# Performance work log

Hardware: AMD Instinct MI355X
Metric: run time of the kernel (lower is better)

Reference implementation:

```python
import jax, jax.numpy as jnp
import numpy as np

S, D_MODEL, H, D_K, D_V = 2048, 1024, 16, 64, 64


def setup_inputs() -> dict:
    key = jax.random.key(0)
    ks = jax.random.split(key, 10)
    sd = 0.02
    return {
        "embeddings": jax.random.normal(ks[0], (S, D_MODEL), dtype=jnp.float32),
        # per-head projection weights (torch Linear: y = x @ W.T + b; here stored as [h, d_in, d_out])
        "Wq": jax.random.normal(ks[1], (H, D_MODEL, D_K), dtype=jnp.float32) * sd,
        "bq": jax.random.normal(ks[2], (H, D_K), dtype=jnp.float32) * sd,
        "Wk": jax.random.normal(ks[3], (H, D_MODEL, D_K), dtype=jnp.float32) * sd,
        "bk": jax.random.normal(ks[4], (H, D_K), dtype=jnp.float32) * sd,
        "Wv": jax.random.normal(ks[5], (H, D_MODEL, D_V), dtype=jnp.float32) * sd,
        "bv": jax.random.normal(ks[6], (H, D_V), dtype=jnp.float32) * sd,
        "Wo": jax.random.normal(ks[7], (H * D_V, D_MODEL), dtype=jnp.float32) * sd,
        "bo": jax.random.normal(ks[8], (D_MODEL,), dtype=jnp.float32) * sd,
    }


def reference(embeddings, Wq, bq, Wk, bk, Wv, bv, Wo, bo):
    # Batched equivalent of the per-head Python loop of ScaledDotProductAttention layers.
    # q,k: [h, s, d_k]; v: [h, s, d_v]
    q = jnp.einsum('sd,hdk->hsk', embeddings, Wq) + bq[:, None, :]
    k = jnp.einsum('sd,hdk->hsk', embeddings, Wk) + bk[:, None, :]
    v = jnp.einsum('sd,hdv->hsv', embeddings, Wv) + bv[:, None, :]
    scale = jnp.asarray(1.0 / np.sqrt(q.shape[-1]), q.dtype)
    scores = jnp.einsum('hsk,htk->hst', q, k) * scale  # [h, s, s]
    attn = jax.nn.softmax(scores, axis=-1)
    heads = jnp.einsum('hst,htv->hsv', attn, v)  # [h, s, d_v]
    # torch.cat(results, dim=1): head outputs concatenated along feature dim -> [s, h*d_v]
    concat = jnp.transpose(heads, (1, 0, 2)).reshape(embeddings.shape[0], -1)
    return concat @ Wo + bo
```

## Files before the change

### kernel.cpp

```cpp
#include <hip/hip_runtime.h>
#include <hip/hip_bf16.h>

typedef unsigned short u16;
typedef __attribute__((ext_vector_type(8))) short bf16x8;
typedef __attribute__((ext_vector_type(4))) float f32x4;

#define S_LEN 2048
#define NH 16

__device__ __forceinline__ u16 f2bf(float x) {
  union { float f; unsigned u; } v; v.f = x;
  unsigned r = v.u + 0x7fffu + ((v.u >> 16) & 1u);
  return (u16)(r >> 16);
}

__device__ __forceinline__ unsigned cvtpk_bf16(float lo, float hi) {
  unsigned w;
  asm("v_cvt_pk_bf16_f32 %0, %1, %2" : "=v"(w) : "v"(lo), "v"(hi));
  return w;
}

__device__ __forceinline__ void async16(const void* g, void* l) {
  __builtin_amdgcn_global_load_lds(
      (const __attribute__((address_space(1))) unsigned int*)g,
      (__attribute__((address_space(3))) unsigned int*)l, 16, 0, 0);
}

__device__ __forceinline__ f32x4 mfma16(bf16x8 a, bf16x8 b, f32x4 c) {
  return __builtin_amdgcn_mfma_f32_16x16x32_bf16(a, b, c, 0, 0, 0);
}

#define QSCALE (0.125f * 1.44269504089f)

__global__ __launch_bounds__(256) void convert_kernel(
    const float* __restrict__ emb, const float* __restrict__ Wq,
    const float* __restrict__ Wk, const float* __restrict__ Wv,
    const float* __restrict__ bq, const float* __restrict__ bk,
    const float* __restrict__ bv, const float* __restrict__ Wo,
    u16* __restrict__ emb_bf, u16* __restrict__ wqkv_t,
    u16* __restrict__ wo_t, float* __restrict__ bqkv) {
  __shared__ float lds[64][65];
  const int b = blockIdx.x, tid = threadIdx.x;
  if (b < 2048) {
    int i = b * 1024 + tid * 4;
    float4 v = *(const float4*)(emb + i);
    ushort4 o = {f2bf(v.x), f2bf(v.y), f2bf(v.z), f2bf(v.w)};
    *(ushort4*)(emb_bf + i) = o;
    return;
  }
  if (b < 2816) {
    int tt = b - 2048;
    int kind = tt >> 8;
    int rem = tt & 255;
    int h = rem >> 4, k0 = (rem & 15) << 6;
    const float* W = (kind == 0) ? Wq : ((kind == 1) ? Wk : Wv);
    const float* src = W + ((size_t)h * 1024 + k0) * 64;
#pragma unroll
    for (int rr = 0; rr < 4; ++rr) {
      int k = rr * 16 + (tid >> 4);
      int d4 = (tid & 15) << 2;
      float4 v = *(const float4*)(src + (size_t)k * 64 + d4);
      lds[k][d4] = v.x; lds[k][d4 + 1] = v.y;
      lds[k][d4 + 2] = v.z; lds[k][d4 + 3] = v.w;
    }
    __syncthreads();
    float scale = (kind == 0) ? QSCALE : 1.f;
#pragma unroll
    for (int p = 0; p < 2; ++p) {
      int d = p * 32 + (tid >> 3);
      int kb = (tid & 7) << 3;
      bf16x8 o;
#pragma unroll
      for (int j = 0; j < 8; ++j) o[j] = (short)f2bf(lds[kb + j][d] * scale);
      *(bf16x8*)(wqkv_t + (size_t)(kind * 1024 + h * 64 + d) * 1024 + k0 + kb) = o;
    }
    return;
  }
  if (b < 3072) {
    int tt = b - 2816;
    int k0 = (tt >> 4) << 6, n0 = (tt & 15) << 6;
#pragma unroll
    for (int rr = 0; rr < 4; ++rr) {
      int k = rr * 16 + (tid >> 4);
      int n4 = (tid & 15) << 2;
      float4 v = *(const float4*)(Wo + (size_t)(k0 + k) * 1024 + n0 + n4);
      lds[k][n4] = v.x; lds[k][n4 + 1] = v.y;
      lds[k][n4 + 2] = v.z; lds[k][n4 + 3] = v.w;
    }
    __syncthreads();
#pragma unroll
    for (int p = 0; p < 2; ++p) {
      int nrel = p * 32 + (tid >> 3);
      int kb = (tid & 7) << 3;
      bf16x8 o;
#pragma unroll
      for (int j = 0; j < 8; ++j) o[j] = (short)f2bf(lds[kb + j][nrel]);
      *(bf16x8*)(wo_t + (size_t)(n0 + nrel) * 1024 + k0 + kb) = o;
    }
    return;
  }
  for (int i = tid; i < 3072; i += 256) {
    int kind = i >> 10, hd = i & 1023;
    const float* bb = (kind == 0) ? bq : ((kind == 1) ? bk : bv);
    float v = bb[hd];
    bqkv[i] = (kind == 0) ? v * QSCALE : v;
  }
}

template <int WM, int WN, int FM, int FN, int BK, bool OUT_BF16, bool VT_SPLIT>
__global__ __launch_bounds__(WM * WN * 64) void gemm_kernel(
    const u16* __restrict__ A, const u16* __restrict__ BT,
    const float* __restrict__ bias, void* __restrict__ Cout,
    u16* __restrict__ vt, int M, int N, int K) {
  constexpr int BM = WM * FM * 16, BN = WN * FN * 16, T = WM * WN * 64;
  constexpr int RB = BK * 2;
  __shared__ u16 lds[2][(BM + BN) * BK];
  const int tid = threadIdx.x;
  const int lane = tid & 63, wave = tid >> 6;
  const int wr = wave / WN, wc = wave % WN;
  const int m0 = blockIdx.x * BM, n0 = blockIdx.y * BN;
  const int r = lane & 15, g = lane >> 4;
  const f32x4 fzero = {0.f, 0.f, 0.f, 0.f};
  f32x4 acc[FM][FN];
#pragma unroll
  for (int i = 0; i < FM; ++i)
#pragma unroll
    for (int j = 0; j < FN; ++j) acc[i][j] = fzero;

  constexpr int LA = (BM * RB) / (T * 16);
  constexpr int LB = (BN * RB) / (T * 16);

  auto stage = [&](int kt, int buf) {
    int k0 = kt * BK;
#pragma unroll
    for (int i = 0; i < LA; ++i) {
      int flat = i * T * 16 + tid * 16;
      int row = flat / RB, colb = flat % RB;
      async16((const char*)A + ((size_t)(m0 + row) * K + k0) * 2 + colb,
              (char*)lds[buf] + i * T * 16 + wave * 1024);
    }
#pragma unroll
    for (int i = 0; i < LB; ++i) {
      int flat = i * T * 16 + tid * 16;
      int row = flat / RB, colb = flat % RB;
      async16((const char*)BT + ((size_t)(n0 + row) * K + k0) * 2 + colb,
              (char*)lds[buf] + BM * RB + i * T * 16 + wave * 1024);
    }
  };

  stage(0, 0);
  asm volatile("s_waitcnt vmcnt(0)" ::: "memory");
  __syncthreads();

  const int NT = K / BK;
  for (int kt = 0; kt < NT; ++kt) {
    int cur = kt & 1;
    if (kt + 1 < NT) stage(kt + 1, cur ^ 1);
    const u16* Al = lds[cur];
    const u16* Bl = Al + BM * BK;
#pragma unroll
    for (int kk = 0; kk < BK / 32; ++kk) {
      bf16x8 af[FM], bfr[FN];
#pragma unroll
      for (int i = 0; i < FM; ++i)
        af[i] = *(const bf16x8*)&Al[(wr * FM * 16 + i * 16 + r) * BK + kk * 32 + g * 8];
#pragma unroll
      for (int j = 0; j < FN; ++j)
        bfr[j] = *(const bf16x8*)&Bl[(wc * FN * 16 + j * 16 + r) * BK + kk * 32 + g * 8];
#pragma unroll
      for (int i = 0; i < FM; ++i)
#pragma unroll
        for (int j = 0; j < FN; ++j)
          acc[i][j] = mfma16(af[i], bfr[j], acc[i][j]);
    }
    asm volatile("s_waitcnt vmcnt(0)" ::: "memory");
    __syncthreads();
  }

  if constexpr (VT_SPLIT) {
    if (n0 >= 2048) {
      int h = (n0 - 2048) >> 6;
#pragma unroll
      for (int i = 0; i < FM; ++i)
#pragma unroll
        for (int j = 0; j < FN; ++j) {
          int d = wc * FN * 16 + j * 16 + r;
          int s0 = m0 + wr * FM * 16 + i * 16 + g * 4;
          float bval = bias[n0 + (d & 63)];
          ushort4 o = {f2bf(acc[i][j][0] + bval), f2bf(acc[i][j][1] + bval),
                       f2bf(acc[i][j][2] + bval), f2bf(acc[i][j][3] + bval)};
          *(ushort4*)(vt + (size_t)h * 131072 + (size_t)d * 2048 + s0) = o;
        }
      return;
    }
  }

#pragma unroll
  for (int i = 0; i < FM; ++i)
#pragma unroll
    for (int j = 0; j < FN; ++j)
#pragma unroll
      for (int e = 0; e < 4; ++e) {
        int row = m0 + wr * FM * 16 + i * 16 + g * 4 + e;
        int col = n0 + wc * FN * 16 + j * 16 + r;
        float v = acc[i][j][e] + bias[col];
        if constexpr (OUT_BF16)
          ((u16*)Cout)[(size_t)row * N + col] = f2bf(v);
        else
          ((float*)Cout)[(size_t)row * N + col] = v;
      }
}

__global__ __launch_bounds__(256) void attn_kernel(const u16* __restrict__ qkv,
                                                   const u16* __restrict__ vt,
                                                   u16* __restrict__ concat) {
  __shared__ __align__(16) char smem[81920];
  const int tid = threadIdx.x;
  const int lane = tid & 63, wave = tid >> 6;
  const int qg = wave >> 1, kvw = wave & 1;
  const int h = blockIdx.y;
  const int q0w = blockIdx.x * 64 + qg * 32;
  const int r = lane & 15, g = lane >> 4;
  const f32x4 fzero = {0.f, 0.f, 0.f, 0.f};
  char* Pw = smem + 65536 + wave * 4096;

  bf16x8 aq[2][2];
#pragma unroll
  for (int qi = 0; qi < 2; ++qi)
#pragma unroll
    for (int kk = 0; kk < 2; ++kk)
      aq[qi][kk] = *(const bf16x8*)&qkv[(size_t)(q0w + qi * 16 + r) * 3072 +
                                        h * 64 + kk * 32 + g * 8];

  f32x4 acc[4][2];
#pragma unroll
  for (int nt = 0; nt < 4; ++nt)
#pragma unroll
    for (int qi = 0; qi < 2; ++qi) acc[nt][qi] = fzero;
  float rs[2] = {0.f, 0.f};

  auto stage = [&](int step) {
    int par = step & 1;
    int t0 = step * 128;
#pragma unroll
    for (int i = 0; i < 4; ++i) {
      int flat = i * 4096 + tid * 16;
      int row = flat >> 7;
      int blk = ((flat >> 4) & 7) ^ (row & 7);
      const char* srcK = (const char*)qkv +
                         ((size_t)(t0 + row) * 3072 + 1024 + h * 64) * 2 + blk * 16;
      async16(srcK, smem + par * 16384 + i * 4096 + wave * 1024);
      int c = row >> 6, d = row & 63;
      const char* srcV = (const char*)vt +
                         ((size_t)h * 131072 + (size_t)d * 2048 + t0 + c * 64) * 2 + blk * 16;
      async16(srcV, smem + 32768 + par * 16384 + i * 4096 + wave * 1024);
    }
  };

  stage(0);
  asm volatile("s_waitcnt vmcnt(0)" ::: "memory");
  __syncthreads();

  for (int step = 0; step < 16; ++step) {
    if (step + 1 < 16) stage(step + 1);
    const int par = step & 1;
    const char* Kb = smem + par * 16384 + kvw * 8192;
    const char* Vb = smem + 32768 + par * 16384 + kvw * 8192;

    f32x4 sv[4][2];
    __builtin_amdgcn_s_setprio(1);
#pragma unroll
    for (int nt = 0; nt < 4; ++nt) {
      sv[nt][0] = fzero;
      sv[nt][1] = fzero;
#pragma unroll
      for (int kk = 0; kk < 2; ++kk) {
        int row = nt * 16 + r;
        const bf16x8 bk = *(const bf16x8*)(Kb + row * 128 +
                                           ((((kk << 2) | g) ^ (row & 7)) << 4));
        sv[nt][0] = mfma16(bk, aq[0][kk], sv[nt][0]);
        sv[nt][1] = mfma16(bk, aq[1][kk], sv[nt][1]);
      }
    }
    __builtin_amdgcn_s_setprio(0);

#pragma unroll
    for (int nt = 0; nt < 4; ++nt)
#pragma unroll
      for (int qi = 0; qi < 2; ++qi) {
        float p0 = exp2f(sv[nt][qi][0]), p1 = exp2f(sv[nt][qi][1]);
        float p2 = exp2f(sv[nt][qi][2]), p3 = exp2f(sv[nt][qi][3]);
        rs[qi] += (p0 + p1) + (p2 + p3);
        uint2 w = {cvtpk_bf16(p0, p1), cvtpk_bf16(p2, p3)};
        int q = qi * 16 + r;
        int off = (q * 128 + nt * 32 + g * 8) ^ ((q & 7) << 4);
        *(uint2*)(Pw + off) = w;
      }

    asm volatile("s_waitcnt lgkmcnt(0)" ::: "memory");
    __builtin_amdgcn_sched_barrier(0);
    bf16x8 pa[2][2];
#pragma unroll
    for (int qi = 0; qi < 2; ++qi)
#pragma unroll
      for (int tc = 0; tc < 2; ++tc) {
        int q = qi * 16 + r;
        pa[qi][tc] = *(const bf16x8*)(Pw + ((q * 128 + tc * 64 + g * 16) ^ ((q & 7) << 4)));
      }
    __builtin_amdgcn_s_setprio(1);
#pragma unroll
    for (int nt = 0; nt < 4; ++nt)
#pragma unroll
      for (int tc = 0; tc < 2; ++tc) {
        int d = (nt << 4) | r;
        const bf16x8 bv = *(const bf16x8*)(Vb + d * 128 +
                                           ((((tc << 2) | g) ^ (d & 7)) << 4));
        acc[nt][0] = mfma16(pa[0][tc], bv, acc[nt][0]);
        acc[nt][1] = mfma16(pa[1][tc], bv, acc[nt][1]);
      }
    __builtin_amdgcn_s_setprio(0);
    asm volatile("s_waitcnt vmcnt(0)" ::: "memory");
    __syncthreads();
  }

#pragma unroll
  for (int qi = 0; qi < 2; ++qi) {
    rs[qi] += __shfl_xor(rs[qi], 16, 64);
    rs[qi] += __shfl_xor(rs[qi], 32, 64);
  }

  float* Ox = (float*)smem;
  float* Lx = (float*)(smem + 64 * 65 * 4);
  if (kvw == 1) {
#pragma unroll
    for (int nt = 0; nt < 4; ++nt)
#pragma unroll
      for (int qi = 0; qi < 2; ++qi)
#pragma unroll
        for (int e = 0; e < 4; ++e) {
          int qb = qg * 32 + qi * 16 + (g << 2) + e;
          Ox[qb * 65 + (nt << 4) + r] = acc[nt][qi][e];
        }
    if (g == 0) {
      Lx[qg * 32 + r] = rs[0];
      Lx[qg * 32 + 16 + r] = rs[1];
    }
  }
  __syncthreads();
  if (kvw == 0) {
#pragma unroll
    for (int qi = 0; qi < 2; ++qi) {
      float inv[4];
#pragma unroll
      for (int e = 0; e < 4; ++e) {
        float own = __shfl(rs[qi], (g << 2) | e, 64);
        inv[e] = 1.f / (own + Lx[qg * 32 + qi * 16 + (g << 2) + e]);
      }
#pragma unroll
      for (int nt = 0; nt < 4; ++nt)
#pragma unroll
        for (int e = 0; e < 4; ++e) {
          int qb = qg * 32 + qi * 16 + (g << 2) + e;
          float o = acc[nt][qi][e] + Ox[qb * 65 + (nt << 4) + r];
          concat[(size_t)(blockIdx.x * 64 + qb) * 1024 + h * 64 + (nt << 4) + r] =
              f2bf(o * inv[e]);
        }
    }
  }
}

extern "C" void kernel_launch(void* const* d_in, const int* in_sizes, int n_in,
                              void* d_out, int out_size, void* d_ws,
                              size_t ws_size, hipStream_t stream) {
  (void)in_sizes; (void)n_in; (void)out_size; (void)ws_size;
  const float* emb = (const float*)d_in[0];
  const float* Wq = (const float*)d_in[1];
  const float* bq = (const float*)d_in[2];
  const float* Wk = (const float*)d_in[3];
  const float* bk = (const float*)d_in[4];
  const float* Wv = (const float*)d_in[5];
  const float* bv = (const float*)d_in[6];
  const float* Wo = (const float*)d_in[7];
  const float* bo = (const float*)d_in[8];

  char* ws = (char*)d_ws;
  u16* emb_bf  = (u16*)(ws + 0);
  u16* wqkv_t  = (u16*)(ws + 4194304);
  u16* wo_t    = (u16*)(ws + 10485760);
  float* bqkv  = (float*)(ws + 12582912);
  u16* qkv     = (u16*)(ws + 12595200);
  u16* vt      = (u16*)(ws + 25178112);
  u16* concat  = (u16*)(ws + 29372416);

  convert_kernel<<<3073, 256, 0, stream>>>(emb, Wq, Wk, Wv, bq, bk, bv, Wo,
                                           emb_bf, wqkv_t, wo_t, bqkv);
  gemm_kernel<2, 2, 4, 2, 64, true, true><<<dim3(16, 48), 256, 0, stream>>>(
      emb_bf, wqkv_t, bqkv, qkv, vt, 2048, 3072, 1024);
  attn_kernel<<<dim3(32, 16), 256, 0, stream>>>(qkv, vt, concat);
  gemm_kernel<2, 2, 2, 2, 64, false, false><<<dim3(32, 16), 256, 0, stream>>>(
      concat, wo_t, bo, d_out, nullptr, 2048, 1024, 1024);
}
```

Baseline: 86.01 us.

## Split attention KV tile across four waves and pass P via ds_bpermute

The attention kernel now runs 512 threads per block, with four waves per query group each taking a 32-key slice of every 128-key tile instead of two waves taking 64 keys each. The softmax probabilities are moved from MFMA output layout to A-operand layout with ds_bpermute lane shuffles instead of a round trip through a per-wave LDS scratch buffer. This removes 16KB of LDS and one wait per step. V is staged with a 16-slot swizzle, and the final reduction now combines three partial accumulators and row sums. The aim is more waves in flight and less LDS traffic per step, at the cost of more cross-wave reduction work and more bpermute instructions.

Result: no change. 84.61 us (-1.6%).

```diff
diff --git a/kernel.cpp b/kernel.cpp
--- a/kernel.cpp
+++ b/kernel.cpp
@@ -211,18 +211,20 @@
       }
 }
 
-__global__ __launch_bounds__(256) void attn_kernel(const u16* __restrict__ qkv,
+__global__ __launch_bounds__(512) void attn_kernel(const u16* __restrict__ qkv,
                                                    const u16* __restrict__ vt,
                                                    u16* __restrict__ concat) {
-  __shared__ __align__(16) char smem[81920];
+  __shared__ __align__(16) char smem[65536];
   const int tid = threadIdx.x;
   const int lane = tid & 63, wave = tid >> 6;
-  const int qg = wave >> 1, kvw = wave & 1;
+  const int qg = wave >> 2, kvw = wave & 3;
   const int h = blockIdx.y;
   const int q0w = blockIdx.x * 64 + qg * 32;
   const int r = lane & 15, g = lane >> 4;
+  const bool hi = (lane & 32) != 0;
+  const int sa0 = (((lane & 16) << 1) | r) << 2;
+  const int sa1 = sa0 + 64;
   const f32x4 fzero = {0.f, 0.f, 0.f, 0.f};
-  char* Pw = smem + 65536 + wave * 4096;
 
   bf16x8 aq[2][2];
 #pragma unroll
@@ -243,17 +245,18 @@
     int par = step & 1;
     int t0 = step * 128;
 #pragma unroll
-    for (int i = 0; i < 4; ++i) {
-      int flat = i * 4096 + tid * 16;
-      int row = flat >> 7;
-      int blk = ((flat >> 4) & 7) ^ (row & 7);
-      const char* srcK = (const char*)qkv +
-                         ((size_t)(t0 + row) * 3072 + 1024 + h * 64) * 2 + blk * 16;
-      async16(srcK, smem + par * 16384 + i * 4096 + wave * 1024);
-      int c = row >> 6, d = row & 63;
-      const char* srcV = (const char*)vt +
-                         ((size_t)h * 131072 + (size_t)d * 2048 + t0 + c * 64) * 2 + blk * 16;
-      async16(srcV, smem + 32768 + par * 16384 + i * 4096 + wave * 1024);
+    for (int i = 0; i < 2; ++i) {
+      int flat = i * 8192 + tid * 16;
+      int krow = flat >> 7;
+      int kslot = ((flat >> 4) & 7) ^ (krow & 7);
+      async16((const char*)qkv +
+                  ((size_t)(t0 + krow) * 3072 + 1024 + h * 64) * 2 + kslot * 16,
+              smem + par * 16384 + flat);
+      int vd = flat >> 8;
+      int vslot = ((flat >> 4) & 15) ^ (vd & 15);
+      async16((const char*)vt +
+                  ((size_t)h * 131072 + (size_t)vd * 2048 + t0 + vslot * 8) * 2,
+              smem + 32768 + par * 16384 + flat);
     }
   };
 
@@ -264,18 +267,18 @@
   for (int step = 0; step < 16; ++step) {
     if (step + 1 < 16) stage(step + 1);
     const int par = step & 1;
-    const char* Kb = smem + par * 16384 + kvw * 8192;
-    const char* Vb = smem + 32768 + par * 16384 + kvw * 8192;
-
-    f32x4 sv[4][2];
+    const char* Kb = smem + par * 16384;
+    const char* Vb = smem + 32768 + par * 16384;
+
+    f32x4 sv[2][2];
     __builtin_amdgcn_s_setprio(1);
 #pragma unroll
-    for (int nt = 0; nt < 4; ++nt) {
+    for (int nt = 0; nt < 2; ++nt) {
       sv[nt][0] = fzero;
       sv[nt][1] = fzero;
+      int row = kvw * 32 + nt * 16 + r;
 #pragma unroll
       for (int kk = 0; kk < 2; ++kk) {
-        int row = nt * 16 + r;
         const bf16x8 bk = *(const bf16x8*)(Kb + row * 128 +
                                            ((((kk << 2) | g) ^ (row & 7)) << 4));
         sv[nt][0] = mfma16(bk, aq[0][kk], sv[nt][0]);
@@ -284,40 +287,42 @@
     }
     __builtin_amdgcn_s_setprio(0);
 
-#pragma unroll
-    for (int nt = 0; nt < 4; ++nt)
+    int w_[2][2][2];
+#pragma unroll
+    for (int nt = 0; nt < 2; ++nt)
 #pragma unroll
       for (int qi = 0; qi < 2; ++qi) {
         float p0 = exp2f(sv[nt][qi][0]), p1 = exp2f(sv[nt][qi][1]);
         float p2 = exp2f(sv[nt][qi][2]), p3 = exp2f(sv[nt][qi][3]);
         rs[qi] += (p0 + p1) + (p2 + p3);
-        uint2 w = {cvtpk_bf16(p0, p1), cvtpk_bf16(p2, p3)};
-        int q = qi * 16 + r;
-        int off = (q * 128 + nt * 32 + g * 8) ^ ((q & 7) << 4);
-        *(uint2*)(Pw + off) = w;
+        w_[nt][qi][0] = (int)cvtpk_bf16(p0, p1);
+        w_[nt][qi][1] = (int)cvtpk_bf16(p2, p3);
       }
 
-    asm volatile("s_waitcnt lgkmcnt(0)" ::: "memory");
-    __builtin_amdgcn_sched_barrier(0);
-    bf16x8 pa[2][2];
-#pragma unroll
-    for (int qi = 0; qi < 2; ++qi)
-#pragma unroll
-      for (int tc = 0; tc < 2; ++tc) {
-        int q = qi * 16 + r;
-        pa[qi][tc] = *(const bf16x8*)(Pw + ((q * 128 + tc * 64 + g * 16) ^ ((q & 7) << 4)));
-      }
+    bf16x8 pa[2];
+#pragma unroll
+    for (int qi = 0; qi < 2; ++qi) {
+      int a0 = __builtin_amdgcn_ds_bpermute(sa0, w_[0][qi][0]);
+      int a1 = __builtin_amdgcn_ds_bpermute(sa0, w_[1][qi][0]);
+      int b0 = __builtin_amdgcn_ds_bpermute(sa0, w_[0][qi][1]);
+      int b1 = __builtin_amdgcn_ds_bpermute(sa0, w_[1][qi][1]);
+      int c0 = __builtin_amdgcn_ds_bpermute(sa1, w_[0][qi][0]);
+      int c1 = __builtin_amdgcn_ds_bpermute(sa1, w_[1][qi][0]);
+      int d0 = __builtin_amdgcn_ds_bpermute(sa1, w_[0][qi][1]);
+      int d1 = __builtin_amdgcn_ds_bpermute(sa1, w_[1][qi][1]);
+      int4 u = {hi ? a1 : a0, hi ? b1 : b0, hi ? c1 : c0, hi ? d1 : d0};
+      pa[qi] = *(bf16x8*)&u;
+    }
+
     __builtin_amdgcn_s_setprio(1);
 #pragma unroll
-    for (int nt = 0; nt < 4; ++nt)
-#pragma unroll
-      for (int tc = 0; tc < 2; ++tc) {
-        int d = (nt << 4) | r;
-        const bf16x8 bv = *(const bf16x8*)(Vb + d * 128 +
-                                           ((((tc << 2) | g) ^ (d & 7)) << 4));
-        acc[nt][0] = mfma16(pa[0][tc], bv, acc[nt][0]);
-        acc[nt][1] = mfma16(pa[1][tc], bv, acc[nt][1]);
-      }
+    for (int nt = 0; nt < 4; ++nt) {
+      int d = nt * 16 + r;
+      const bf16x8 bv = *(const bf16x8*)(Vb + d * 256 +
+                                         ((((kvw << 2) | g) ^ (d & 15)) << 4));
+      acc[nt][0] = mfma16(pa[0], bv, acc[nt][0]);
+      acc[nt][1] = mfma16(pa[1], bv, acc[nt][1]);
+    }
     __builtin_amdgcn_s_setprio(0);
     asm volatile("s_waitcnt vmcnt(0)" ::: "memory");
     __syncthreads();
@@ -330,8 +335,9 @@
   }
 
   float* Ox = (float*)smem;
-  float* Lx = (float*)(smem + 64 * 65 * 4);
-  if (kvw == 1) {
+  float* Lx = (float*)(smem + 49920);
+  if (kvw != 0) {
+    int kb = kvw - 1;
 #pragma unroll
     for (int nt = 0; nt < 4; ++nt)
 #pragma unroll
@@ -339,11 +345,11 @@
 #pragma unroll
         for (int e = 0; e < 4; ++e) {
           int qb = qg * 32 + qi * 16 + (g << 2) + e;
-          Ox[qb * 65 + (nt << 4) + r] = acc[nt][qi][e];
+          Ox[kb * 4160 + qb * 65 + nt * 16 + r] = acc[nt][qi][e];
         }
     if (g == 0) {
-      Lx[qg * 32 + r] = rs[0];
-      Lx[qg * 32 + 16 + r] = rs[1];
+      Lx[kb * 64 + qg * 32 + r] = rs[0];
+      Lx[kb * 64 + qg * 32 + 16 + r] = rs[1];
     }
   }
   __syncthreads();
@@ -353,16 +359,19 @@
       float inv[4];
 #pragma unroll
       for (int e = 0; e < 4; ++e) {
+        int qb = qg * 32 + qi * 16 + (g << 2) + e;
         float own = __shfl(rs[qi], (g << 2) | e, 64);
-        inv[e] = 1.f / (own + Lx[qg * 32 + qi * 16 + (g << 2) + e]);
+        inv[e] = 1.f / (own + Lx[qb] + Lx[64 + qb] + Lx[128 + qb]);
       }
 #pragma unroll
       for (int nt = 0; nt < 4; ++nt)
 #pragma unroll
         for (int e = 0; e < 4; ++e) {
           int qb = qg * 32 + qi * 16 + (g << 2) + e;
-          float o = acc[nt][qi][e] + Ox[qb * 65 + (nt << 4) + r];
-          concat[(size_t)(blockIdx.x * 64 + qb) * 1024 + h * 64 + (nt << 4) + r] =
+          int d = nt * 16 + r;
+          float o = acc[nt][qi][e] + Ox[qb * 65 + d] + Ox[4160 + qb * 65 + d] +
+                    Ox[8320 + qb * 65 + d];
+          concat[(size_t)(blockIdx.x * 64 + qb) * 1024 + h * 64 + d] =
               f2bf(o * inv[e]);
         }
     }
@@ -396,7 +405,7 @@
                                            emb_bf, wqkv_t, wo_t, bqkv);
   gemm_kernel<2, 2, 4, 2, 64, true, true><<<dim3(16, 48), 256, 0, stream>>>(
       emb_bf, wqkv_t, bqkv, qkv, vt, 2048, 3072, 1024);
-  attn_kernel<<<dim3(32, 16), 256, 0, stream>>>(qkv, vt, concat);
+  attn_kernel<<<dim3(32, 16), 512, 0, stream>>>(qkv, vt, concat);
   gemm_kernel<2, 2, 2, 2, 64, false, false><<<dim3(32, 16), 256, 0, stream>>>(
       concat, wo_t, bo, d_out, nullptr, 2048, 1024, 1024);
 }
```
